# Performance work log

Measured on AMD Instinct MI355X. Metric: run time of the kernel, lower is better.

Reference implementation:

```python
import jax, jax.numpy as jnp
import numpy as np

L1, L2, B, D = 512, 512, 32, 768
EPS = 1e-8

def setup_inputs() -> dict:
    key = jax.random.key(0)
    k1, k2 = jax.random.split(key)
    return {
        "x1": jax.random.normal(k1, (L1, B, D), dtype=jnp.float32),
        "x1_mask": jnp.ones((L1, B), dtype=jnp.float32),
        "x2": jax.random.normal(k2, (L2, B, D), dtype=jnp.float32),
        "x2_mask": jnp.ones((L2, B), dtype=jnp.float32),
    }

def reference(x1, x1_mask, x2, x2_mask):
    # to batch-major: [B, L, D]
    x1b = jnp.transpose(x1, (1, 0, 2))
    x2b = jnp.transpose(x2, (1, 0, 2))
    m1 = jnp.transpose(x1_mask, (1, 0))  # [B, L1]
    m2 = jnp.transpose(x2_mask, (1, 0))  # [B, L2]

    # raw scores [B, L1, L2]
    scores = jnp.einsum('bld,bmd->blm', x1b, x2b)

    # x1 attends over x2: softmax over axis 2 with x2 mask
    w2 = jnp.exp(scores - jnp.max(scores, axis=2, keepdims=True))
    w2 = w2 * m2[:, None, :]
    alpha = w2 / (jnp.sum(w2, axis=-1, keepdims=True) + EPS)  # [B, L1, L2]
    x1_dual = jnp.einsum('blm,bmd->bld', alpha, x2b)           # [B, L1, D]

    # x2 attends over x1: stabilize with max over axis 1, then transpose
    w1 = jnp.exp(scores - jnp.max(scores, axis=1, keepdims=True))
    w1 = jnp.transpose(w1, (0, 2, 1))                          # [B, L2, L1]
    w1 = w1 * m1[:, None, :]
    beta = w1 / (jnp.sum(w1, axis=-1, keepdims=True) + EPS)    # [B, L2, L1]
    x2_dual = jnp.einsum('bml,bld->bmd', beta, x1b)            # [B, L2, D]

    # back to seq-major [L, B, D]
    return (jnp.transpose(x1_dual, (1, 0, 2)), jnp.transpose(x2_dual, (1, 0, 2)))
```

## Files before the change

kernel.cpp:

```cpp
#include <hip/hip_runtime.h>

#define LQ  512
#define LKN 512
#define BB  32
#define DD  768
#define DSL (DD / 4)

typedef float    f4     __attribute__((ext_vector_type(4)));
typedef _Float16 half8  __attribute__((ext_vector_type(8)));
typedef _Float16 half4  __attribute__((ext_vector_type(4)));
typedef __fp16   fp16x2 __attribute__((ext_vector_type(2)));

union H8 { half8 h; unsigned int u[4]; };

__device__ __forceinline__ unsigned int pk2(float a, float b) {
    union { fp16x2 h; unsigned int u; } c;
    c.h = __builtin_amdgcn_cvt_pkrtz(a, b);
    return c.u;
}
__device__ __forceinline__ half8 cvt8(f4 a, f4 b) {
    H8 r;
    r.u[0] = pk2(a[0], a[1]); r.u[1] = pk2(a[2], a[3]);
    r.u[2] = pk2(b[0], b[1]); r.u[3] = pk2(b[2], b[3]);
    return r.h;
}

__device__ __forceinline__ void gload16(half8& dst, const _Float16* p) {
    asm volatile("global_load_dwordx4 %0, %1, off" : "=v"(dst) : "v"(p));
}

__global__ __launch_bounds__(256)
void prep_cvt_t(const float* __restrict__ x1, const float* __restrict__ x2,
                _Float16* __restrict__ xf1, _Float16* __restrict__ xf2,
                _Float16* __restrict__ xv1, _Float16* __restrict__ xv2)
{
    const int bi   = blockIdx.x;
    const int side = bi / 3072;
    const int rem  = bi % 3072;
    const int b    = rem / 96;
    const int rem2 = rem % 96;
    const int l0   = (rem2 / 12) * 64;
    const int d0   = (rem2 % 12) * 64;

    const float* __restrict__ X  = side ? x2  : x1;
    _Float16* __restrict__    XF = side ? xf2 : xf1;
    _Float16* __restrict__    XV = side ? xv2 : xv1;

    __shared__ _Float16 T[64][72];

    const int tid = threadIdx.x;
    {
        const int r  = tid >> 4;
        const int c4 = (tid & 15) * 4;
        for (int rr = r; rr < 64; rr += 16) {
            const size_t idx = ((size_t)(l0 + rr) * BB + b) * DD + d0 + c4;
            f4 v = *(const f4*)(X + idx);
            half4 h;
            h[0] = (_Float16)v[0]; h[1] = (_Float16)v[1];
            h[2] = (_Float16)v[2]; h[3] = (_Float16)v[3];
            *(half4*)&T[rr][c4] = h;
        }
    }
    __syncthreads();
    #pragma unroll
    for (int c = tid; c < 512; c += 256) {
        const int t16l = c >> 7;
        const int ksl  = (c >> 6) & 1;
        const int ln   = c & 63;
        half8 v = *(const half8*)&T[t16l * 16 + (ln & 15)][ksl * 32 + (ln >> 4) * 8];
        const size_t t16g = (size_t)(l0 >> 4) + t16l;
        const size_t ksg  = (size_t)(d0 >> 5) + ksl;
        *(half8*)(XF + (((size_t)b * 32 + t16g) * 24 + ksg) * 512 + ln * 8) = v;
    }
    #pragma unroll
    for (int c = tid; c < 512; c += 256) {
        const int dtl  = c >> 7;
        const int ks2l = (c >> 6) & 1;
        const int ln   = c & 63;
        half8 v;
        #pragma unroll
        for (int jj = 0; jj < 8; ++jj)
            v[jj] = T[ks2l * 32 + (ln >> 4) * 8 + jj][dtl * 16 + (ln & 15)];
        *(half8*)(XV + (((size_t)b * 48 + (d0 >> 4) + dtl) * 16 + (l0 >> 5) + ks2l) * 512 + ln * 8) = v;
    }
}

__global__ __launch_bounds__(256, 3)
void gemm_s(const _Float16* __restrict__ xf1, const _Float16* __restrict__ xf2,
            float* __restrict__ S)
{
    const int i   = blockIdx.x;
    const int xcd = i & 7;
    const int j   = i >> 3;
    const int t   = j & 15;
    const int b   = xcd * 4 + (j >> 4);
    const int lt  = t >> 2, mt = t & 3;
    const int l0b = lt * 128, m0b = mt * 128;

    const int tid  = threadIdx.x;
    const int lane = tid & 63;
    const int w    = tid >> 6;
    const int wl   = w >> 1, wm = w & 1;
    const int lr   = lane & 15;
    const int lg   = lane >> 4;

    f4 acc[16];
    #pragma unroll
    for (int t2 = 0; t2 < 16; ++t2) acc[t2] = f4{0.f, 0.f, 0.f, 0.f};

    {
        const _Float16* ab = xf1 + (((size_t)b * 32 + lt * 8 + wl * 4) * 24) * 512 + lane * 8;
        const _Float16* bb = xf2 + (((size_t)b * 32 + mt * 8 + wm * 4) * 24) * 512 + lane * 8;
        __builtin_amdgcn_s_setprio(1);
        #pragma unroll
        for (int ks = 0; ks < 24; ++ks) {
            half8 aF[4], bF[4];
            #pragma unroll
            for (int q = 0; q < 4; ++q) {
                aF[q] = *(const half8*)(ab + ((size_t)q * 24 + ks) * 512);
                bF[q] = *(const half8*)(bb + ((size_t)q * 24 + ks) * 512);
            }
            #pragma unroll
            for (int q = 0; q < 4; ++q)
                #pragma unroll
                for (int p = 0; p < 4; ++p)
                    acc[q * 4 + p] = __builtin_amdgcn_mfma_f32_16x16x32_f16(aF[q], bF[p], acc[q * 4 + p], 0, 0, 0);
        }
        __builtin_amdgcn_s_setprio(0);
    }

    {
        float* srow = S + ((size_t)b * 512 + l0b + wl * 64) * 512 + m0b + wm * 64;
        #pragma unroll
        for (int q = 0; q < 4; ++q)
            #pragma unroll
            for (int p = 0; p < 4; ++p)
                #pragma unroll
                for (int r = 0; r < 4; ++r)
                    srow[(size_t)(q * 16 + 4 * lg + r) * 512 + p * 16 + lr] = acc[q * 4 + p][r];
    }
}

__global__ __launch_bounds__(256)
void transpose_s(const float* __restrict__ S, float* __restrict__ ST)
{
    const int i   = blockIdx.x;
    const int xcd = i & 7;
    const int j   = i >> 3;
    const int t   = j & 63;
    const int b   = xcd * 4 + (j >> 6);
    const int lt  = t >> 3, mt = t & 7;

    __shared__ float T[64][65];

    const int tid = threadIdx.x;
    const int r   = tid >> 2;
    const int c0  = (tid & 3) * 16;

    {
        const float* src = S + ((size_t)b * 512 + lt * 64 + r) * 512 + mt * 64 + c0;
        #pragma unroll
        for (int k = 0; k < 4; ++k) {
            f4 v = *(const f4*)(src + k * 4);
            T[r][c0 + k * 4 + 0] = v[0]; T[r][c0 + k * 4 + 1] = v[1];
            T[r][c0 + k * 4 + 2] = v[2]; T[r][c0 + k * 4 + 3] = v[3];
        }
    }
    __syncthreads();
    {
        float* dst = ST + ((size_t)b * 512 + mt * 64 + r) * 512 + lt * 64 + c0;
        #pragma unroll
        for (int k = 0; k < 4; ++k) {
            f4 v;
            v[0] = T[c0 + k * 4 + 0][r]; v[1] = T[c0 + k * 4 + 1][r];
            v[2] = T[c0 + k * 4 + 2][r]; v[3] = T[c0 + k * 4 + 3][r];
            *(f4*)(dst + k * 4) = v;
        }
    }
}

__global__ __launch_bounds__(256)
void softmax_pf(float* __restrict__ S32, float* __restrict__ ST32,
                const float* __restrict__ m1, const float* __restrict__ m2)
{
    const int bi   = blockIdx.x;
    const int side = bi >> 9;
    const int idx  = bi & 511;
    const int b    = idx >> 4;
    const int rt   = idx & 15;

    float* __restrict__ P = side ? ST32 : S32;
    const float* __restrict__ MK = side ? m1 : m2;

    const int tid  = threadIdx.x;
    const int lane = tid & 63;
    const int w    = tid >> 6;

    __shared__ float mask_s[LKN];
    mask_s[tid] = MK[tid * BB + b];
    mask_s[tid + 256] = MK[(tid + 256) * BB + b];
    __syncthreads();

    float mk[8];
    #pragma unroll
    for (int j = 0; j < 8; ++j) mk[j] = mask_s[lane * 8 + j];

    const int row0 = rt * 32 + w * 8;

    f4 fa[8], fb[8];
    #pragma unroll
    for (int rr = 0; rr < 8; ++rr) {
        const float* rp = P + ((size_t)b * 512 + row0 + rr) * 512 + lane * 8;
        fa[rr] = *(const f4*)rp;
        fb[rr] = *(const f4*)(rp + 4);
    }

    H8 outw[8];
    #pragma unroll
    for (int rr = 0; rr < 8; ++rr) {
        float f[8] = {fa[rr][0], fa[rr][1], fa[rr][2], fa[rr][3],
                      fb[rr][0], fb[rr][1], fb[rr][2], fb[rr][3]};
        float m = fmaxf(fmaxf(fmaxf(f[0], f[1]), fmaxf(f[2], f[3])),
                        fmaxf(fmaxf(f[4], f[5]), fmaxf(f[6], f[7])));
        #pragma unroll
        for (int d = 1; d <= 32; d <<= 1) m = fmaxf(m, __shfl_xor(m, d));
        float e[8], s = 0.f;
        #pragma unroll
        for (int j = 0; j < 8; ++j) { e[j] = __expf(f[j] - m) * mk[j]; s += e[j]; }
        #pragma unroll
        for (int d = 1; d <= 32; d <<= 1) s += __shfl_xor(s, d);
        const float inv = 1.f / (s + 1e-8f);
        outw[rr].u[0] = pk2(e[0] * inv, e[1] * inv);
        outw[rr].u[1] = pk2(e[2] * inv, e[3] * inv);
        outw[rr].u[2] = pk2(e[4] * inv, e[5] * inv);
        outw[rr].u[3] = pk2(e[6] * inv, e[7] * inv);
    }

    __syncthreads();

    #pragma unroll
    for (int rr = 0; rr < 8; ++rr) {
        const int row = row0 + rr;
        char* base = (char*)P + ((size_t)b * 512 + (size_t)(row >> 4) * 16) * 2048;
        char* dst  = base + (lane >> 2) * 1024 + (lane & 3) * 256 + (row & 15) * 16;
        *(half8*)dst = outw[rr].h;
    }
}

__global__ __launch_bounds__(256)
void pv_frag(const float* __restrict__ S32, const float* __restrict__ ST32,
             const _Float16* __restrict__ xv1, const _Float16* __restrict__ xv2,
             float* __restrict__ o1, float* __restrict__ o2)
{
    const int i    = blockIdx.x;
    const int xcd  = i & 7;
    const int j    = i >> 3;
    const int lt   = j & 7;
    const int dq   = (j >> 3) & 3;
    const int side = (j >> 5) & 1;
    const int b    = xcd * 4 + (j >> 6);
    const int l0   = lt * 64;

    const float* __restrict__ P32   = side ? ST32 : S32;
    const _Float16* __restrict__ VF = side ? xv1 : xv2;
    float* __restrict__ OUT         = side ? o2 : o1;

    const int tid  = threadIdx.x;
    const int lane = tid & 63;
    const int w    = tid >> 6;
    const int lr   = lane & 15;
    const int lg   = lane >> 4;

    const char* pb[4];
    #pragma unroll
    for (int q = 0; q < 4; ++q)
        pb[q] = (const char*)P32 + ((size_t)b * 512 + (size_t)(lt * 4 + q) * 16) * 2048 + lane * 16;
    const _Float16* vbase = VF + (((size_t)b * 48 + dq * 12 + w * 3) * 16) * 512 + lane * 8;

    f4 acc[12];
    #pragma unroll
    for (int t = 0; t < 12; ++t) acc[t] = f4{0.f, 0.f, 0.f, 0.f};

    #pragma unroll
    for (int cb = 0; cb < 8; ++cb) {
        half8 pa[2][4], vf[2][3];
        #pragma unroll
        for (int k2 = 0; k2 < 2; ++k2) {
            const int ks2 = cb * 2 + k2;
            #pragma unroll
            for (int q = 0; q < 4; ++q)
                gload16(pa[k2][q], (const _Float16*)(pb[q] + ks2 * 1024));
            #pragma unroll
            for (int nt = 0; nt < 3; ++nt)
                gload16(vf[k2][nt], vbase + ((size_t)nt * 16 + ks2) * 512);
        }
        asm volatile("s_waitcnt vmcnt(0)" ::: "memory");
        __builtin_amdgcn_sched_barrier(0);
        __builtin_amdgcn_s_setprio(1);
        #pragma unroll
        for (int k2 = 0; k2 < 2; ++k2)
            #pragma unroll
            for (int nt = 0; nt < 3; ++nt)
                #pragma unroll
                for (int q = 0; q < 4; ++q)
                    acc[q * 3 + nt] = __builtin_amdgcn_mfma_f32_16x16x32_f16(pa[k2][q], vf[k2][nt], acc[q * 3 + nt], 0, 0, 0);
        __builtin_amdgcn_s_setprio(0);
    }

    #pragma unroll
    for (int q = 0; q < 4; ++q)
        #pragma unroll
        for (int nt = 0; nt < 3; ++nt)
            #pragma unroll
            for (int r = 0; r < 4; ++r)
                OUT[((size_t)(l0 + q * 16 + 4 * lg + r) * BB + b) * DD + dq * 192 + (w * 3 + nt) * 16 + lr]
                    = acc[q * 3 + nt][r];
}

__global__ __launch_bounds__(256)
void coatt_flash_f32(const float* __restrict__ x1, const float* __restrict__ m1,
                     const float* __restrict__ x2, const float* __restrict__ m2,
                     float* __restrict__ o1, float* __restrict__ o2)
{
    const int i    = blockIdx.x;
    const int xcd  = i & 7;
    const int j    = i >> 3;
    const int pair = xcd * 8 + (j >> 5);
    const int qt   = j & 31;
    const int side = pair >> 5;
    const int b    = pair & 31;

    const float* __restrict__ Q   = side ? x2 : x1;
    const float* __restrict__ K   = side ? x1 : x2;
    const float* __restrict__ MK  = side ? m1 : m2;
    float* __restrict__       OUT = side ? o2 : o1;

    const int tid  = threadIdx.x;
    const int lane = tid & 63;
    const int w    = tid >> 6;
    const int lr   = lane & 15;
    const int lg   = lane >> 4;
    const int q0 = qt * 16;
    const int d0 = w * DSL;

    __shared__ float sred[4][16][36];
    __shared__ float mask_s[LKN];
    for (int t = tid; t < LKN; t += 256) mask_s[t] = MK[t * BB + b];

    half8 qf[6];
    {
        const float* qrow = Q + ((q0 + lr) * BB + b) * DD + d0 + lg * 8;
        #pragma unroll
        for (int ks = 0; ks < 6; ++ks) {
            f4 a = *(const f4*)(qrow + ks * 32);
            f4 c = *(const f4*)(qrow + ks * 32 + 4);
            qf[ks] = cvt8(a, c);
        }
    }
    f4 acc[12];
    #pragma unroll
    for (int t = 0; t < 12; ++t) acc[t] = f4{0.f, 0.f, 0.f, 0.f};
    float Mrun = -3.0e38f, Lrun = 0.f;
    for (int kt = 0; kt < 16; ++kt) {
        const int k0 = kt * 32;
        f4 s0 = {0.f,0.f,0.f,0.f}, s1 = {0.f,0.f,0.f,0.f};
        {
            const float* kb0 = K + ((k0 + lr) * BB + b) * DD + d0 + lg * 8;
            const float* kb1 = kb0 + 16 * BB * DD;
            #pragma unroll
            for (int ks = 0; ks < 6; ++ks) {
                f4 a0 = *(const f4*)(kb0 + ks * 32);
                f4 c0 = *(const f4*)(kb0 + ks * 32 + 4);
                s0 = __builtin_amdgcn_mfma_f32_16x16x32_f16(qf[ks], cvt8(a0, c0), s0, 0, 0, 0);
                f4 a1 = *(const f4*)(kb1 + ks * 32);
                f4 c1 = *(const f4*)(kb1 + ks * 32 + 4);
                s1 = __builtin_amdgcn_mfma_f32_16x16x32_f16(qf[ks], cvt8(a1, c1), s1, 0, 0, 0);
            }
        }
        __syncthreads();
        #pragma unroll
        for (int r = 0; r < 4; ++r) {
            sred[w][4 * lg + r][lr]      = s0[r];
            sred[w][4 * lg + r][16 + lr] = s1[r];
        }
        __syncthreads();
        f4 sa = {0.f,0.f,0.f,0.f}, sb = {0.f,0.f,0.f,0.f};
        #pragma unroll
        for (int ww = 0; ww < 4; ++ww) {
            sa += *(const f4*)&sred[ww][lr][lg * 8];
            sb += *(const f4*)&sred[ww][lr][lg * 8 + 4];
        }
        float tmax = fmaxf(fmaxf(fmaxf(sa[0], sa[1]), fmaxf(sa[2], sa[3])),
                           fmaxf(fmaxf(sb[0], sb[1]), fmaxf(sb[2], sb[3])));
        tmax = fmaxf(tmax, __shfl_xor(tmax, 16));
        tmax = fmaxf(tmax, __shfl_xor(tmax, 32));
        const float Mnew  = fmaxf(Mrun, tmax);
        const float scale = __expf(Mrun - Mnew);
        float p[8];
        float psum = 0.f;
        const float* mrow = &mask_s[k0 + lg * 8];
        #pragma unroll
        for (int t = 0; t < 4; ++t) { p[t]     = __expf(sa[t] - Mnew) * mrow[t];     psum += p[t]; }
        #pragma unroll
        for (int t = 0; t < 4; ++t) { p[4 + t] = __expf(sb[t] - Mnew) * mrow[4 + t]; psum += p[4 + t]; }
        psum += __shfl_xor(psum, 16);
        psum += __shfl_xor(psum, 32);
        Lrun = Lrun * scale + psum;
        Mrun = Mnew;
        H8 pf;
        pf.u[0] = pk2(p[0], p[1]); pf.u[1] = pk2(p[2], p[3]);
        pf.u[2] = pk2(p[4], p[5]); pf.u[3] = pk2(p[6], p[7]);
        float sc[4];
        #pragma unroll
        for (int r = 0; r < 4; ++r) sc[r] = __shfl(scale, (lane & 48) + 4 * lg + r);
        #pragma unroll
        for (int t = 0; t < 12; ++t) {
            acc[t][0] *= sc[0]; acc[t][1] *= sc[1];
            acc[t][2] *= sc[2]; acc[t][3] *= sc[3];
        }
        const float* vb = K + ((k0 + lg * 8) * BB + b) * DD + d0 + lr;
        #pragma unroll
        for (int nt = 0; nt < 12; ++nt) {
            const float* vp = vb + nt * 16;
            float vv[8];
            #pragma unroll
            for (int t = 0; t < 8; ++t) vv[t] = vp[t * BB * DD];
            H8 vf;
            vf.u[0] = pk2(vv[0], vv[1]); vf.u[1] = pk2(vv[2], vv[3]);
            vf.u[2] = pk2(vv[4], vv[5]); vf.u[3] = pk2(vv[6], vv[7]);
            acc[nt] = __builtin_amdgcn_mfma_f32_16x16x32_f16(pf.h, vf.h, acc[nt], 0, 0, 0);
        }
    }
    float il[4];
    {
        const float inv = 1.f / (Lrun + 1e-8f);
        #pragma unroll
        for (int r = 0; r < 4; ++r) il[r] = __shfl(inv, (lane & 48) + 4 * lg + r);
    }
    #pragma unroll
    for (int nt = 0; nt < 12; ++nt) {
        #pragma unroll
        for (int r = 0; r < 4; ++r) {
            OUT[((q0 + 4 * lg + r) * BB + b) * DD + d0 + nt * 16 + lr] = acc[nt][r] * il[r];
        }
    }
}

extern "C" void kernel_launch(void* const* d_in, const int* in_sizes, int n_in,
                              void* d_out, int out_size, void* d_ws, size_t ws_size,
                              hipStream_t stream) {
    (void)in_sizes; (void)n_in; (void)out_size;
    const float* x1 = (const float*)d_in[0];
    const float* m1 = (const float*)d_in[1];
    const float* x2 = (const float*)d_in[2];
    const float* m2 = (const float*)d_in[3];
    float* o1 = (float*)d_out;
    float* o2 = o1 + (size_t)LQ * BB * DD;

    const size_t ELEMS = (size_t)LQ * BB * DD;
    const size_t SELEM = (size_t)BB * 512 * 512;
    const size_t NEED  = 4 * ELEMS * sizeof(_Float16)
                       + SELEM * sizeof(float);

    if (ws_size >= NEED) {
        _Float16* xf1 = (_Float16*)d_ws;
        _Float16* xf2 = xf1 + ELEMS;
        _Float16* xv1 = xf2 + ELEMS;
        _Float16* xv2 = xv1 + ELEMS;
        float*    S32 = (float*)(xv2 + ELEMS);
        float*    ST32 = (float*)d_ws;
        prep_cvt_t<<<6144, 256, 0, stream>>>(x1, x2, xf1, xf2, xv1, xv2);
        gemm_s<<<512, 256, 0, stream>>>(xf1, xf2, S32);
        transpose_s<<<2048, 256, 0, stream>>>(S32, ST32);
        softmax_pf<<<1024, 256, 0, stream>>>(S32, ST32, m1, m2);
        pv_frag<<<2048, 256, 0, stream>>>(S32, ST32, xv1, xv2, o1, o2);
    } else {
        coatt_flash_f32<<<2048, 256, 0, stream>>>(x1, m1, x2, m2, o1, o2);
    }
}
```

Baseline: 159.4 us.

## Fuse score transpose into column softmax and widen prep conversion tiles

The separate transpose kernel, which wrote a full transposed fp32 score matrix, is removed. A new column-softmax kernel reads column strips of S directly, transposes them through shared memory, computes max and sum per column, and writes packed fp16 fragments for the second attention side. This saves one full fp32 read and write of the score tensor. The prep kernel now processes 128-wide D tiles with batched asm loads, halving the block count. The column kernel uses about 66KB of LDS per block, which limits occupancy. Its serial per-thread column loops may also be slower than the old row-wise softmax.

```diff
diff --git a/kernel.cpp b/kernel.cpp
--- a/kernel.cpp
+++ b/kernel.cpp
@@ -28,60 +28,77 @@
 __device__ __forceinline__ void gload16(half8& dst, const _Float16* p) {
     asm volatile("global_load_dwordx4 %0, %1, off" : "=v"(dst) : "v"(p));
 }
+__device__ __forceinline__ void gloadf4(f4& dst, const float* p) {
+    asm volatile("global_load_dwordx4 %0, %1, off" : "=v"(dst) : "v"(p));
+}
 
 __global__ __launch_bounds__(256)
-void prep_cvt_t(const float* __restrict__ x1, const float* __restrict__ x2,
-                _Float16* __restrict__ xf1, _Float16* __restrict__ xf2,
-                _Float16* __restrict__ xv1, _Float16* __restrict__ xv2)
+void prep_pack(const float* __restrict__ x1, const float* __restrict__ x2,
+               _Float16* __restrict__ xf1, _Float16* __restrict__ xf2,
+               _Float16* __restrict__ xv1, _Float16* __restrict__ xv2)
 {
     const int bi   = blockIdx.x;
-    const int side = bi / 3072;
-    const int rem  = bi % 3072;
-    const int b    = rem / 96;
-    const int rem2 = rem % 96;
-    const int l0   = (rem2 / 12) * 64;
-    const int d0   = (rem2 % 12) * 64;
+    const int side = bi / 1536;
+    const int rem  = bi % 1536;
+    const int b    = rem / 48;
+    const int rem2 = rem % 48;
+    const int l0   = (rem2 / 6) * 64;
+    const int d0   = (rem2 % 6) * 128;
 
     const float* __restrict__ X  = side ? x2  : x1;
     _Float16* __restrict__    XF = side ? xf2 : xf1;
     _Float16* __restrict__    XV = side ? xv2 : xv1;
 
-    __shared__ _Float16 T[64][72];
+    __shared__ _Float16 T[64][136];
 
     const int tid = threadIdx.x;
     {
         const int r  = tid >> 4;
-        const int c4 = (tid & 15) * 4;
-        for (int rr = r; rr < 64; rr += 16) {
-            const size_t idx = ((size_t)(l0 + rr) * BB + b) * DD + d0 + c4;
-            f4 v = *(const f4*)(X + idx);
-            half4 h;
-            h[0] = (_Float16)v[0]; h[1] = (_Float16)v[1];
-            h[2] = (_Float16)v[2]; h[3] = (_Float16)v[3];
-            *(half4*)&T[rr][c4] = h;
+        const int c8 = (tid & 15) * 8;
+        const float* src = X + ((size_t)(l0 + r) * BB + b) * DD + d0 + c8;
+        f4 v[8];
+        #pragma unroll
+        for (int k = 0; k < 4; ++k) {
+            gloadf4(v[2 * k],     src + (size_t)k * 16 * BB * DD);
+            gloadf4(v[2 * k + 1], src + (size_t)k * 16 * BB * DD + 4);
+        }
+        asm volatile("s_waitcnt vmcnt(0)" ::: "memory");
+        __builtin_amdgcn_sched_barrier(0);
+        #pragma unroll
+        for (int k = 0; k < 4; ++k) {
+            half4 ha, hb;
+            ha[0] = (_Float16)v[2*k][0]; ha[1] = (_Float16)v[2*k][1];
+            ha[2] = (_Float16)v[2*k][2]; ha[3] = (_Float16)v[2*k][3];
+            hb[0] = (_Float16)v[2*k+1][0]; hb[1] = (_Float16)v[2*k+1][1];
+            hb[2] = (_Float16)v[2*k+1][2]; hb[3] = (_Float16)v[2*k+1][3];
+            *(half4*)&T[r + 16 * k][c8]     = ha;
+            *(half4*)&T[r + 16 * k][c8 + 4] = hb;
         }
     }
     __syncthreads();
     #pragma unroll
-    for (int c = tid; c < 512; c += 256) {
-        const int t16l = c >> 7;
-        const int ksl  = (c >> 6) & 1;
-        const int ln   = c & 63;
-        half8 v = *(const half8*)&T[t16l * 16 + (ln & 15)][ksl * 32 + (ln >> 4) * 8];
+    for (int c2 = tid; c2 < 1024; c2 += 256) {
+        const int dhalf = c2 >> 9;
+        const int t16l  = (c2 >> 7) & 3;
+        const int ksl   = (c2 >> 6) & 1;
+        const int ln    = c2 & 63;
+        half8 v = *(const half8*)&T[t16l * 16 + (ln & 15)][dhalf * 64 + ksl * 32 + (ln >> 4) * 8];
         const size_t t16g = (size_t)(l0 >> 4) + t16l;
-        const size_t ksg  = (size_t)(d0 >> 5) + ksl;
+        const size_t ksg  = (size_t)(d0 >> 5) + dhalf * 2 + ksl;
         *(half8*)(XF + (((size_t)b * 32 + t16g) * 24 + ksg) * 512 + ln * 8) = v;
     }
     #pragma unroll
-    for (int c = tid; c < 512; c += 256) {
-        const int dtl  = c >> 7;
-        const int ks2l = (c >> 6) & 1;
-        const int ln   = c & 63;
+    for (int c2 = tid; c2 < 1024; c2 += 256) {
+        const int dtl  = c2 >> 7;
+        const int ks2l = (c2 >> 6) & 1;
+        const int ln   = c2 & 63;
         half8 v;
         #pragma unroll
         for (int jj = 0; jj < 8; ++jj)
             v[jj] = T[ks2l * 32 + (ln >> 4) * 8 + jj][dtl * 16 + (ln & 15)];
-        *(half8*)(XV + (((size_t)b * 48 + (d0 >> 4) + dtl) * 16 + (l0 >> 5) + ks2l) * 512 + ln * 8) = v;
+        const size_t dtg  = (size_t)(d0 >> 4) + dtl;
+        const size_t ks2g = (size_t)(l0 >> 5) + ks2l;
+        *(half8*)(XV + (((size_t)b * 48 + dtg) * 16 + ks2g) * 512 + ln * 8) = v;
     }
 }
 
@@ -142,63 +159,107 @@
 }
 
 __global__ __launch_bounds__(256)
-void transpose_s(const float* __restrict__ S, float* __restrict__ ST)
+void softmax_col_pf(const float* __restrict__ S32, float* __restrict__ PF1,
+                    const float* __restrict__ m1)
 {
-    const int i   = blockIdx.x;
-    const int xcd = i & 7;
-    const int j   = i >> 3;
-    const int t   = j & 63;
-    const int b   = xcd * 4 + (j >> 6);
-    const int lt  = t >> 3, mt = t & 7;
-
-    __shared__ float T[64][65];
+    const int i  = blockIdx.x;
+    const int b  = i >> 4;
+    const int ct = i & 15;
 
     const int tid = threadIdx.x;
-    const int r   = tid >> 2;
-    const int c0  = (tid & 3) * 16;
+
+    __shared__ float raw[32][513];
+    __shared__ float mask_s[LKN];
+    __shared__ float redm[8][32];
+    __shared__ float reds[8][32];
+
+    mask_s[tid] = m1[tid * BB + b];
+    mask_s[tid + 256] = m1[(tid + 256) * BB + b];
 
     {
-        const float* src = S + ((size_t)b * 512 + lt * 64 + r) * 512 + mt * 64 + c0;
-        #pragma unroll
-        for (int k = 0; k < 4; ++k) {
-            f4 v = *(const f4*)(src + k * 4);
-            T[r][c0 + k * 4 + 0] = v[0]; T[r][c0 + k * 4 + 1] = v[1];
-            T[r][c0 + k * 4 + 2] = v[2]; T[r][c0 + k * 4 + 3] = v[3];
+        const float* sbase = S32 + ((size_t)b * 512 + (tid >> 3)) * 512 + ct * 32 + (tid & 7) * 4;
+        f4 vv[16];
+        #pragma unroll
+        for (int it = 0; it < 8; ++it) gloadf4(vv[it], sbase + (size_t)it * 32 * 512);
+        asm volatile("s_waitcnt vmcnt(0)" ::: "memory");
+        __builtin_amdgcn_sched_barrier(0);
+        #pragma unroll
+        for (int it = 8; it < 16; ++it) gloadf4(vv[it], sbase + (size_t)it * 32 * 512);
+        #pragma unroll
+        for (int it = 0; it < 8; ++it) {
+            const int row = it * 32 + (tid >> 3);
+            const int c0  = (tid & 7) * 4;
+            raw[c0 + 0][row] = vv[it][0]; raw[c0 + 1][row] = vv[it][1];
+            raw[c0 + 2][row] = vv[it][2]; raw[c0 + 3][row] = vv[it][3];
+        }
+        asm volatile("s_waitcnt vmcnt(0)" ::: "memory");
+        __builtin_amdgcn_sched_barrier(0);
+        #pragma unroll
+        for (int it = 8; it < 16; ++it) {
+            const int row = it * 32 + (tid >> 3);
+            const int c0  = (tid & 7) * 4;
+            raw[c0 + 0][row] = vv[it][0]; raw[c0 + 1][row] = vv[it][1];
+            raw[c0 + 2][row] = vv[it][2]; raw[c0 + 3][row] = vv[it][3];
         }
     }
     __syncthreads();
-    {
-        float* dst = ST + ((size_t)b * 512 + mt * 64 + r) * 512 + lt * 64 + c0;
-        #pragma unroll
-        for (int k = 0; k < 4; ++k) {
-            f4 v;
-            v[0] = T[c0 + k * 4 + 0][r]; v[1] = T[c0 + k * 4 + 1][r];
-            v[2] = T[c0 + k * 4 + 2][r]; v[3] = T[c0 + k * 4 + 3][r];
-            *(f4*)(dst + k * 4) = v;
-        }
+
+    const int col = tid & 31;
+    const int seg = tid >> 5;
+
+    float m = -3.0e38f;
+    #pragma unroll
+    for (int r = 0; r < 64; ++r) m = fmaxf(m, raw[col][seg * 64 + r]);
+    redm[seg][col] = m;
+    __syncthreads();
+    float M = redm[0][col];
+    #pragma unroll
+    for (int s2 = 1; s2 < 8; ++s2) M = fmaxf(M, redm[s2][col]);
+
+    float s = 0.f;
+    #pragma unroll
+    for (int r = 0; r < 64; ++r) {
+        const int row = seg * 64 + r;
+        s += __expf(raw[col][row] - M) * mask_s[row];
+    }
+    reds[seg][col] = s;
+    __syncthreads();
+    float L = 0.f;
+    #pragma unroll
+    for (int s2 = 0; s2 < 8; ++s2) L += reds[s2][col];
+    const float inv = 1.f / (L + 1e-8f);
+
+    const int col_g = ct * 32 + col;
+    char* pfb = (char*)PF1 + ((size_t)b * 512 + (size_t)(col_g >> 4) * 16) * 2048;
+    #pragma unroll
+    for (int kc = 0; kc < 8; ++kc) {
+        const int k0 = seg * 64 + kc * 8;
+        float e[8];
+        #pragma unroll
+        for (int j = 0; j < 8; ++j)
+            e[j] = __expf(raw[col][k0 + j] - M) * mask_s[k0 + j] * inv;
+        H8 o;
+        o.u[0] = pk2(e[0], e[1]); o.u[1] = pk2(e[2], e[3]);
+        o.u[2] = pk2(e[4], e[5]); o.u[3] = pk2(e[6], e[7]);
+        const int lane_w = seg * 8 + kc;
+        *(half8*)(pfb + (lane_w >> 2) * 1024 + (lane_w & 3) * 256 + (col_g & 15) * 16) = o.h;
     }
 }
 
 __global__ __launch_bounds__(256)
-void softmax_pf(float* __restrict__ S32, float* __restrict__ ST32,
-                const float* __restrict__ m1, const float* __restrict__ m2)
+void softmax_row_pf(float* __restrict__ S32, const float* __restrict__ m2)
 {
-    const int bi   = blockIdx.x;
-    const int side = bi >> 9;
-    const int idx  = bi & 511;
-    const int b    = idx >> 4;
-    const int rt   = idx & 15;
-
-    float* __restrict__ P = side ? ST32 : S32;
-    const float* __restrict__ MK = side ? m1 : m2;
+    const int i  = blockIdx.x;
+    const int b  = i >> 4;
+    const int rt = i & 15;
 
     const int tid  = threadIdx.x;
     const int lane = tid & 63;
     const int w    = tid >> 6;
 
     __shared__ float mask_s[LKN];
-    mask_s[tid] = MK[tid * BB + b];
-    mask_s[tid + 256] = MK[(tid + 256) * BB + b];
+    mask_s[tid] = m2[tid * BB + b];
+    mask_s[tid + 256] = m2[(tid + 256) * BB + b];
     __syncthreads();
 
     float mk[8];
@@ -210,7 +271,7 @@
     f4 fa[8], fb[8];
     #pragma unroll
     for (int rr = 0; rr < 8; ++rr) {
-        const float* rp = P + ((size_t)b * 512 + row0 + rr) * 512 + lane * 8;
+        const float* rp = S32 + ((size_t)b * 512 + row0 + rr) * 512 + lane * 8;
         fa[rr] = *(const f4*)rp;
         fb[rr] = *(const f4*)(rp + 4);
     }
@@ -241,7 +302,7 @@
     #pragma unroll
     for (int rr = 0; rr < 8; ++rr) {
         const int row = row0 + rr;
-        char* base = (char*)P + ((size_t)b * 512 + (size_t)(row >> 4) * 16) * 2048;
+        char* base = (char*)S32 + ((size_t)b * 512 + (size_t)(row >> 4) * 16) * 2048;
         char* dst  = base + (lane >> 2) * 1024 + (lane & 3) * 256 + (row & 15) * 16;
         *(half8*)dst = outw[rr].h;
     }
@@ -468,12 +529,12 @@
         _Float16* xv1 = xf2 + ELEMS;
         _Float16* xv2 = xv1 + ELEMS;
         float*    S32 = (float*)(xv2 + ELEMS);
-        float*    ST32 = (float*)d_ws;
-        prep_cvt_t<<<6144, 256, 0, stream>>>(x1, x2, xf1, xf2, xv1, xv2);
+        float*    PF1 = (float*)d_ws;
+        prep_pack<<<3072, 256, 0, stream>>>(x1, x2, xf1, xf2, xv1, xv2);
         gemm_s<<<512, 256, 0, stream>>>(xf1, xf2, S32);
-        transpose_s<<<2048, 256, 0, stream>>>(S32, ST32);
-        softmax_pf<<<1024, 256, 0, stream>>>(S32, ST32, m1, m2);
-        pv_frag<<<2048, 256, 0, stream>>>(S32, ST32, xv1, xv2, o1, o2);
+        softmax_col_pf<<<512, 256, 0, stream>>>(S32, PF1, m1);
+        softmax_row_pf<<<512, 256, 0, stream>>>(S32, m2);
+        pv_frag<<<2048, 256, 0, stream>>>(S32, PF1, xv1, xv2, o1, o2);
     } else {
         coatt_flash_f32<<<2048, 256, 0, stream>>>(x1, m1, x2, m2, o1, o2);
     }
```

New measurement: 143.9 us. 1.11x faster.
